# Optimization experiments

Hardware: AMD Instinct MI355X
Metric: run time of the kernel (lower is better)

The kernel has to match this reference:

```python
import jax, jax.numpy as jnp
import numpy as np

B, N, K, F_IN, F_OUT = 8, 2048, 32, 256, 256


def setup_inputs() -> dict:
    key = jax.random.key(0)
    ks = jax.random.split(key, 8)
    x = jax.random.normal(ks[0], (B, N, F_IN), dtype=jnp.float32)
    idx_neib = jax.random.randint(ks[1], (N, K), 0, N, dtype=jnp.int32)
    # Linear params (torch nn.Linear stores weight as [out, in])
    lim_x = np.sqrt(2.0) * np.sqrt(6.0 / (F_IN + F_OUT))  # xavier_uniform, gain=relu
    Wx_w = jax.random.uniform(ks[2], (F_OUT, F_IN), jnp.float32, -lim_x, lim_x)
    Wx_b = jnp.zeros((F_OUT,), jnp.float32)
    Wn_w = jax.random.uniform(ks[3], (F_OUT, F_IN), jnp.float32, -lim_x, lim_x)
    Wn_b = jnp.zeros((F_OUT,), jnp.float32)
    gamma = jnp.ones((2 * F_OUT,), jnp.float32)
    beta = jnp.zeros((2 * F_OUT,), jnp.float32)
    return {"x": x, "idx_neib": idx_neib, "Wx_w": Wx_w, "Wx_b": Wx_b,
            "Wn_w": Wn_w, "Wn_b": Wn_b, "gamma": gamma, "beta": beta}


def reference(x, idx_neib, Wx_w, Wx_b, Wn_w, Wn_b, gamma, beta):
    # Gather neighbor features: [B, N, K, F] then mean over the K neighbors.
    x_neib = jnp.take(x, idx_neib, axis=1).mean(axis=2)  # [B, N, F]
    # Dual linear projections (weights stored [out, in] as in torch).
    h_self = jnp.einsum('bnf,of->bno', x, Wx_w) + Wx_b
    h_nei = jnp.einsum('bnf,of->bno', x_neib, Wn_w) + Wn_b
    h = jnp.concatenate([h_self, h_nei], axis=2)          # [B, N, 2*out]
    # F.normalize(p=2, dim=2): divide by max(||h||_2, 1e-12)
    nrm = jnp.sqrt(jnp.sum(h * h, axis=2, keepdims=True))
    h = h / jnp.maximum(nrm, 1e-12)
    h = jax.nn.relu(h)
    # BatchNorm1d over channel dim (training mode: batch stats over B and N,
    # biased variance), eps=1e-5.
    mu = h.mean(axis=(0, 1))
    var = jnp.mean((h - mu) ** 2, axis=(0, 1))
    h = (h - mu) * jax.lax.rsqrt(var + 1e-5) * gamma + beta
    return h
```

## Files before the change

kernel.cpp:

```cpp
#include <hip/hip_runtime.h>
#include <stdint.h>

#define BB 8
#define NN 2048
#define KK 32
#define FIN 256
#define FOUT 256
#define CC 512
#define MM (BB*NN)
#define RB 32
#define NBLK (MM/RB)
#define LDA 264

typedef __attribute__((ext_vector_type(8))) short short8;
typedef __attribute__((ext_vector_type(4))) float f32x4;

__device__ __forceinline__ unsigned short f2bf(float f) {
    union { float f; unsigned u; } v; v.f = f;
    unsigned u = v.u;
    return (unsigned short)((u + 0x7FFFu + ((u >> 16) & 1u)) >> 16);
}
__device__ __forceinline__ float bf2f(unsigned short s) {
    union { unsigned u; float f; } v; v.u = ((unsigned)s) << 16;
    return v.f;
}

__global__ void k_pre(const float* __restrict__ x, const int* __restrict__ idx,
                      const float* __restrict__ Wx, const float* __restrict__ Wxb,
                      const float* __restrict__ Wn, const float* __restrict__ Wnb,
                      unsigned short* __restrict__ xnb,
                      unsigned short* __restrict__ Wc, float* __restrict__ bc) {
    const int blk = blockIdx.x;
    const int tid = threadIdx.x;
    if (blk < 512) {
        int gid = blk * 256 + tid;
        int o = gid >> 8, k = gid & 255;
        float w = (o < FOUT) ? Wx[o * FIN + k] : Wn[(o - FOUT) * FIN + k];
        Wc[gid] = f2bf(w);
        if (gid < CC) bc[gid] = (gid < FOUT) ? Wxb[gid] : Wnb[gid - FOUT];
    } else {
        int g = blk - 512;
        int b = g & 7;
        int n = (g >> 3) * 4 + (tid >> 6);
        int lane = tid & 63;
        const int* ip = idx + n * KK;
        const float* xp = x + (size_t)b * NN * FIN + lane * 4;
        float a0 = 0.f, a1 = 0.f, a2 = 0.f, a3 = 0.f;
        #pragma unroll 8
        for (int k = 0; k < KK; ++k) {
            float4 v = *(const float4*)(xp + (size_t)ip[k] * FIN);
            a0 += v.x; a1 += v.y; a2 += v.z; a3 += v.w;
        }
        const float s = 1.0f / (float)KK;
        ushort4 o4; o4.x = f2bf(a0 * s); o4.y = f2bf(a1 * s);
        o4.z = f2bf(a2 * s); o4.w = f2bf(a3 * s);
        *(ushort4*)(xnb + ((size_t)b * NN + n) * FIN + lane * 4) = o4;
    }
}

__global__ __launch_bounds__(256, 3)
void k_gemm(const float* __restrict__ x,
            const unsigned short* __restrict__ xnb,
            const unsigned short* __restrict__ Wc,
            const float* __restrict__ bc,
            unsigned short* __restrict__ h,
            float* __restrict__ psum, float* __restrict__ psq) {
    __shared__ unsigned short As[2][RB * LDA];
    __shared__ float sqpart[4][RB];
    __shared__ float rnorm[RB];

    const int tid  = threadIdx.x;
    const int w    = tid >> 6;
    const int lane = tid & 63;
    const int quad = lane >> 4;
    const int l16  = lane & 15;
    const int r0   = blockIdx.x * RB;

    {
        const float4* gs = (const float4*)(x + (size_t)r0 * FIN);
        #pragma unroll
        for (int i = 0; i < 8; ++i) {
            int e = tid + i * 256;
            float4 v = gs[e];
            ushort4 o4; o4.x = f2bf(v.x); o4.y = f2bf(v.y); o4.z = f2bf(v.z); o4.w = f2bf(v.w);
            *(ushort4*)&As[0][(e >> 6) * LDA + (e & 63) * 4] = o4;
        }
    }
    {
        const uint4* gn = (const uint4*)(xnb + (size_t)r0 * FIN);
        #pragma unroll
        for (int i = 0; i < 4; ++i) {
            int e = tid + i * 256;
            *(uint4*)&As[1][(e >> 5) * LDA + (e & 31) * 8] = gn[e];
        }
    }
    __syncthreads();

    const unsigned short* A = As[w >> 1];
    const int cb = w * 128;

    f32x4 acc[2][8];
    #pragma unroll
    for (int mt = 0; mt < 2; ++mt)
        #pragma unroll
        for (int nt = 0; nt < 8; ++nt) acc[mt][nt] = (f32x4){0.f, 0.f, 0.f, 0.f};

    const unsigned short* Bp = Wc + (size_t)(cb + l16) * FIN + quad * 8;
    const unsigned short* Ap = A + (size_t)l16 * LDA + quad * 8;

    #pragma unroll 2
    for (int k0 = 0; k0 < FIN; k0 += 32) {
        short8 a0 = *(const short8*)(Ap + k0);
        short8 a1 = *(const short8*)(Ap + 16 * LDA + k0);
        short8 bfr[8];
        #pragma unroll
        for (int nt = 0; nt < 8; ++nt)
            bfr[nt] = *(const short8*)(Bp + (size_t)nt * 16 * FIN + k0);
        #pragma unroll
        for (int nt = 0; nt < 8; ++nt) {
            acc[0][nt] = __builtin_amdgcn_mfma_f32_16x16x32_bf16(a0, bfr[nt], acc[0][nt], 0, 0, 0);
            acc[1][nt] = __builtin_amdgcn_mfma_f32_16x16x32_bf16(a1, bfr[nt], acc[1][nt], 0, 0, 0);
        }
    }

    float bcv[8];
    #pragma unroll
    for (int nt = 0; nt < 8; ++nt) bcv[nt] = bc[cb + nt * 16 + l16];

    float rsq[2][4] = {{0.f,0.f,0.f,0.f},{0.f,0.f,0.f,0.f}};
    #pragma unroll
    for (int mt = 0; mt < 2; ++mt)
        #pragma unroll
        for (int nt = 0; nt < 8; ++nt)
            #pragma unroll
            for (int r = 0; r < 4; ++r) {
                float v = acc[mt][nt][r] + bcv[nt];
                acc[mt][nt][r] = v;
                rsq[mt][r] += v * v;
            }
    #pragma unroll
    for (int off = 1; off < 16; off <<= 1)
        #pragma unroll
        for (int mt = 0; mt < 2; ++mt)
            #pragma unroll
            for (int r = 0; r < 4; ++r)
                rsq[mt][r] += __shfl_xor(rsq[mt][r], off, 64);
    if (l16 == 0) {
        #pragma unroll
        for (int mt = 0; mt < 2; ++mt)
            #pragma unroll
            for (int r = 0; r < 4; ++r)
                sqpart[w][mt * 16 + quad * 4 + r] = rsq[mt][r];
    }
    __syncthreads();
    if (tid < RB) {
        float tot = sqpart[0][tid] + sqpart[1][tid] + sqpart[2][tid] + sqpart[3][tid];
        rnorm[tid] = 1.0f / fmaxf(sqrtf(tot), 1e-12f);
    }
    __syncthreads();

    float csum[8] = {0.f,0.f,0.f,0.f,0.f,0.f,0.f,0.f};
    float csq [8] = {0.f,0.f,0.f,0.f,0.f,0.f,0.f,0.f};
    #pragma unroll
    for (int mt = 0; mt < 2; ++mt) {
        #pragma unroll
        for (int r = 0; r < 4; ++r) {
            int row = mt * 16 + quad * 4 + r;
            float rn = rnorm[row];
            unsigned short* hp = h + (size_t)(r0 + row) * CC + cb + l16;
            #pragma unroll
            for (int nt = 0; nt < 8; ++nt) {
                float v = fmaxf(acc[mt][nt][r] * rn, 0.0f);
                hp[nt * 16] = f2bf(v);
                csum[nt] += v;
                csq [nt] += v * v;
            }
        }
    }
    #pragma unroll
    for (int off = 16; off < 64; off <<= 1)
        #pragma unroll
        for (int nt = 0; nt < 8; ++nt) {
            csum[nt] += __shfl_xor(csum[nt], off, 64);
            csq [nt] += __shfl_xor(csq [nt], off, 64);
        }
    if (quad == 0) {
        #pragma unroll
        for (int nt = 0; nt < 8; ++nt) {
            int c = cb + nt * 16 + l16;
            psum[(size_t)c * NBLK + blockIdx.x] = csum[nt];
            psq [(size_t)c * NBLK + blockIdx.x] = csq [nt];
        }
    }
}

__global__ void k_stats(const float* __restrict__ psum, const float* __restrict__ psq,
                        const float* __restrict__ gamma, const float* __restrict__ beta,
                        float* __restrict__ ss) {
    __shared__ float ps[4], pq[4];
    int c = blockIdx.x, t = threadIdx.x;
    float s = psum[(size_t)c * NBLK + t] + psum[(size_t)c * NBLK + 256 + t];
    float q = psq [(size_t)c * NBLK + t] + psq [(size_t)c * NBLK + 256 + t];
    #pragma unroll
    for (int off = 32; off; off >>= 1) { s += __shfl_xor(s, off, 64); q += __shfl_xor(q, off, 64); }
    int w = t >> 6, lane = t & 63;
    if (lane == 0) { ps[w] = s; pq[w] = q; }
    __syncthreads();
    if (t == 0) {
        float S = ps[0] + ps[1] + ps[2] + ps[3];
        float Q = pq[0] + pq[1] + pq[2] + pq[3];
        const float inv = 1.0f / (float)MM;
        float mu  = S * inv;
        float var = fmaxf(Q * inv - mu * mu, 0.0f);
        float sc  = gamma[c] * rsqrtf(var + 1e-5f);
        ss[c]      = sc;
        ss[CC + c] = beta[c] - mu * sc;
    }
}

__global__ void k_apply(const unsigned short* __restrict__ h,
                        const float* __restrict__ ss,
                        float* __restrict__ out) {
    int gid = blockIdx.x * 256 + threadIdx.x;
    int c0 = (gid * 8) & (CC - 1);
    uint4 hv = ((const uint4*)h)[gid];
    const unsigned short* hs = (const unsigned short*)&hv;
    float4 sc0 = *(const float4*)(ss + c0);
    float4 sc1 = *(const float4*)(ss + c0 + 4);
    float4 sh0 = *(const float4*)(ss + CC + c0);
    float4 sh1 = *(const float4*)(ss + CC + c0 + 4);
    float4 o0, o1;
    o0.x = bf2f(hs[0]) * sc0.x + sh0.x;
    o0.y = bf2f(hs[1]) * sc0.y + sh0.y;
    o0.z = bf2f(hs[2]) * sc0.z + sh0.z;
    o0.w = bf2f(hs[3]) * sc0.w + sh0.w;
    o1.x = bf2f(hs[4]) * sc1.x + sh1.x;
    o1.y = bf2f(hs[5]) * sc1.y + sh1.y;
    o1.z = bf2f(hs[6]) * sc1.z + sh1.z;
    o1.w = bf2f(hs[7]) * sc1.w + sh1.w;
    ((float4*)out)[gid * 2]     = o0;
    ((float4*)out)[gid * 2 + 1] = o1;
}

extern "C" void kernel_launch(void* const* d_in, const int* in_sizes, int n_in,
                              void* d_out, int out_size, void* d_ws, size_t ws_size,
                              hipStream_t stream) {
    const float* x     = (const float*)d_in[0];
    const int*   idx   = (const int*)  d_in[1];
    const float* Wx_w  = (const float*)d_in[2];
    const float* Wx_b  = (const float*)d_in[3];
    const float* Wn_w  = (const float*)d_in[4];
    const float* Wn_b  = (const float*)d_in[5];
    const float* gamma = (const float*)d_in[6];
    const float* beta  = (const float*)d_in[7];
    float* out = (float*)d_out;

    char* p = (char*)d_ws;
    unsigned short* xnb = (unsigned short*)p; p += (size_t)MM * FIN * 2;
    unsigned short* Wc  = (unsigned short*)p; p += (size_t)CC * FIN * 2;
    float* bc           = (float*)p;          p += (size_t)CC * 4;
    unsigned short* h   = (unsigned short*)p; p += (size_t)MM * CC * 2;
    float* psum         = (float*)p;          p += (size_t)CC * NBLK * 4;
    float* psq          = (float*)p;          p += (size_t)CC * NBLK * 4;
    float* ss           = (float*)p;          p += (size_t)2 * CC * 4;

    hipLaunchKernelGGL(k_pre,   dim3(4608), dim3(256), 0, stream,
                       x, idx, Wx_w, Wx_b, Wn_w, Wn_b, xnb, Wc, bc);
    hipLaunchKernelGGL(k_gemm,  dim3(NBLK), dim3(256), 0, stream, x, xnb, Wc, bc, h, psum, psq);
    hipLaunchKernelGGL(k_stats, dim3(CC),   dim3(256), 0, stream, psum, psq, gamma, beta, ss);
    hipLaunchKernelGGL(k_apply, dim3(4096), dim3(256), 0, stream, h, ss, out);
}
```

Before: 139.2 us.

## Fuse neighbor gather-mean into GEMM kernel and vectorize weight prep

The neighbor mean gather moves from the prep kernel into the GEMM kernel, which now builds the bf16 neighbor tile directly in shared memory. This removes the xnb intermediate write and read to global memory. Blocks are renumbered so consecutive blocks share the same node range across batches, which may help L2 reuse of the gathered rows. Weight conversion is vectorized to float4 with fewer blocks. The cost is a heavier GEMM prologue with serial gather latency per block, and launch bounds drop to 2 blocks per SM.

```diff
diff --git a/kernel.cpp b/kernel.cpp
--- a/kernel.cpp
+++ b/kernel.cpp
@@ -25,42 +25,26 @@
     return v.f;
 }
 
-__global__ void k_pre(const float* __restrict__ x, const int* __restrict__ idx,
-                      const float* __restrict__ Wx, const float* __restrict__ Wxb,
-                      const float* __restrict__ Wn, const float* __restrict__ Wnb,
-                      unsigned short* __restrict__ xnb,
-                      unsigned short* __restrict__ Wc, float* __restrict__ bc) {
-    const int blk = blockIdx.x;
-    const int tid = threadIdx.x;
-    if (blk < 512) {
-        int gid = blk * 256 + tid;
-        int o = gid >> 8, k = gid & 255;
-        float w = (o < FOUT) ? Wx[o * FIN + k] : Wn[(o - FOUT) * FIN + k];
-        Wc[gid] = f2bf(w);
-        if (gid < CC) bc[gid] = (gid < FOUT) ? Wxb[gid] : Wnb[gid - FOUT];
-    } else {
-        int g = blk - 512;
-        int b = g & 7;
-        int n = (g >> 3) * 4 + (tid >> 6);
-        int lane = tid & 63;
-        const int* ip = idx + n * KK;
-        const float* xp = x + (size_t)b * NN * FIN + lane * 4;
-        float a0 = 0.f, a1 = 0.f, a2 = 0.f, a3 = 0.f;
-        #pragma unroll 8
-        for (int k = 0; k < KK; ++k) {
-            float4 v = *(const float4*)(xp + (size_t)ip[k] * FIN);
-            a0 += v.x; a1 += v.y; a2 += v.z; a3 += v.w;
-        }
-        const float s = 1.0f / (float)KK;
-        ushort4 o4; o4.x = f2bf(a0 * s); o4.y = f2bf(a1 * s);
-        o4.z = f2bf(a2 * s); o4.w = f2bf(a3 * s);
-        *(ushort4*)(xnb + ((size_t)b * NN + n) * FIN + lane * 4) = o4;
-    }
-}
-
-__global__ __launch_bounds__(256, 3)
-void k_gemm(const float* __restrict__ x,
-            const unsigned short* __restrict__ xnb,
+__global__ void k_prep(const float* __restrict__ Wx, const float* __restrict__ Wxb,
+                       const float* __restrict__ Wn, const float* __restrict__ Wnb,
+                       unsigned short* __restrict__ Wc, float* __restrict__ bc) {
+    int gid = blockIdx.x * 256 + threadIdx.x;
+    int e0 = gid * 4;
+    int o = e0 >> 8, k = e0 & 255;
+    const float* src = (o < FOUT) ? (Wx + o * FIN + k) : (Wn + (o - FOUT) * FIN + k);
+    float4 v = *(const float4*)src;
+    ushort4 p; p.x = f2bf(v.x); p.y = f2bf(v.y); p.z = f2bf(v.z); p.w = f2bf(v.w);
+    *(ushort4*)(Wc + e0) = p;
+    if (gid < 128) {
+        int c0 = gid * 4;
+        float4 bv = (c0 < FOUT) ? *(const float4*)(Wxb + c0)
+                                : *(const float4*)(Wnb + c0 - FOUT);
+        *(float4*)(bc + c0) = bv;
+    }
+}
+
+__global__ __launch_bounds__(256, 2)
+void k_gemm(const float* __restrict__ x, const int* __restrict__ idx,
             const unsigned short* __restrict__ Wc,
             const float* __restrict__ bc,
             unsigned short* __restrict__ h,
@@ -69,15 +53,19 @@
     __shared__ float sqpart[4][RB];
     __shared__ float rnorm[RB];
 
+    const int bid  = blockIdx.x;
     const int tid  = threadIdx.x;
     const int w    = tid >> 6;
     const int lane = tid & 63;
     const int quad = lane >> 4;
     const int l16  = lane & 15;
-    const int r0   = blockIdx.x * RB;
+    const int b    = bid & 7;
+    const int n0   = (bid >> 3) * RB;
+    const float* xbat = x + (size_t)b * NN * FIN;
+    const size_t r0g = (size_t)b * NN + n0;
 
     {
-        const float4* gs = (const float4*)(x + (size_t)r0 * FIN);
+        const float4* gs = (const float4*)(xbat + (size_t)n0 * FIN);
         #pragma unroll
         for (int i = 0; i < 8; ++i) {
             int e = tid + i * 256;
@@ -87,11 +75,21 @@
         }
     }
     {
-        const uint4* gn = (const uint4*)(xnb + (size_t)r0 * FIN);
-        #pragma unroll
-        for (int i = 0; i < 4; ++i) {
-            int e = tid + i * 256;
-            *(uint4*)&As[1][(e >> 5) * LDA + (e & 31) * 8] = gn[e];
+        #pragma unroll
+        for (int rr = 0; rr < 8; ++rr) {
+            int lr = w * 8 + rr;
+            const int* ip = idx + (n0 + lr) * KK;
+            const float* xp = xbat + lane * 4;
+            float a0 = 0.f, a1 = 0.f, a2 = 0.f, a3 = 0.f;
+            #pragma unroll 8
+            for (int k = 0; k < KK; ++k) {
+                float4 v = *(const float4*)(xp + (size_t)ip[k] * FIN);
+                a0 += v.x; a1 += v.y; a2 += v.z; a3 += v.w;
+            }
+            const float s = 1.0f / (float)KK;
+            ushort4 o4; o4.x = f2bf(a0 * s); o4.y = f2bf(a1 * s);
+            o4.z = f2bf(a2 * s); o4.w = f2bf(a3 * s);
+            *(ushort4*)&As[1][lr * LDA + lane * 4] = o4;
         }
     }
     __syncthreads();
@@ -167,7 +165,7 @@
         for (int r = 0; r < 4; ++r) {
             int row = mt * 16 + quad * 4 + r;
             float rn = rnorm[row];
-            unsigned short* hp = h + (size_t)(r0 + row) * CC + cb + l16;
+            unsigned short* hp = h + (r0g + row) * CC + cb + l16;
             #pragma unroll
             for (int nt = 0; nt < 8; ++nt) {
                 float v = fmaxf(acc[mt][nt][r] * rn, 0.0f);
@@ -188,8 +186,8 @@
         #pragma unroll
         for (int nt = 0; nt < 8; ++nt) {
             int c = cb + nt * 16 + l16;
-            psum[(size_t)c * NBLK + blockIdx.x] = csum[nt];
-            psq [(size_t)c * NBLK + blockIdx.x] = csq [nt];
+            psum[(size_t)c * NBLK + bid] = csum[nt];
+            psq [(size_t)c * NBLK + bid] = csq [nt];
         }
     }
 }
@@ -256,17 +254,15 @@
     float* out = (float*)d_out;
 
     char* p = (char*)d_ws;
-    unsigned short* xnb = (unsigned short*)p; p += (size_t)MM * FIN * 2;
-    unsigned short* Wc  = (unsigned short*)p; p += (size_t)CC * FIN * 2;
-    float* bc           = (float*)p;          p += (size_t)CC * 4;
-    unsigned short* h   = (unsigned short*)p; p += (size_t)MM * CC * 2;
-    float* psum         = (float*)p;          p += (size_t)CC * NBLK * 4;
-    float* psq          = (float*)p;          p += (size_t)CC * NBLK * 4;
-    float* ss           = (float*)p;          p += (size_t)2 * CC * 4;
-
-    hipLaunchKernelGGL(k_pre,   dim3(4608), dim3(256), 0, stream,
-                       x, idx, Wx_w, Wx_b, Wn_w, Wn_b, xnb, Wc, bc);
-    hipLaunchKernelGGL(k_gemm,  dim3(NBLK), dim3(256), 0, stream, x, xnb, Wc, bc, h, psum, psq);
+    unsigned short* Wc = (unsigned short*)p; p += (size_t)CC * FIN * 2;
+    float* bc          = (float*)p;          p += (size_t)CC * 4;
+    unsigned short* h  = (unsigned short*)p; p += (size_t)MM * CC * 2;
+    float* psum        = (float*)p;          p += (size_t)CC * NBLK * 4;
+    float* psq         = (float*)p;          p += (size_t)CC * NBLK * 4;
+    float* ss          = (float*)p;          p += (size_t)2 * CC * 4;
+
+    hipLaunchKernelGGL(k_prep,  dim3(128),  dim3(256), 0, stream, Wx_w, Wx_b, Wn_w, Wn_b, Wc, bc);
+    hipLaunchKernelGGL(k_gemm,  dim3(NBLK), dim3(256), 0, stream, x, idx, Wc, bc, h, psum, psq);
     hipLaunchKernelGGL(k_stats, dim3(CC),   dim3(256), 0, stream, psum, psq, gamma, beta, ss);
     hipLaunchKernelGGL(k_apply, dim3(4096), dim3(256), 0, stream, h, ss, out);
 }
```

Measured after the change: 138.6 us. About the same (-0.5%).
